# Optimization experiments

Hardware: AMD Instinct MI355X
Metric: run time of the kernel (lower is better)

## Reference

```python
import jax, jax.numpy as jnp
import numpy as np

T = 1024
H_DIM = 2048
VOCAB = 32000
N_EXPERTS = 8
TOP_K = 2
MOE_I = 1024
SHARED_I = 1024
N_HEADS = 16
Q_LORA = 512
KV_LORA = 256
NOPE = 64
ROPE = 32
V_D = 64
EPS = 1e-6
ROUTED_SCALE = 2.5
NEG = -1e30


def rmsnorm(x, w, eps=EPS):
    return x * jax.lax.rsqrt(jnp.mean(x * x, axis=-1, keepdims=True) + eps) * w


def rope_cos_sin(positions):
    inv_freq = 1.0 / (10000.0 ** (jnp.arange(0, ROPE, 2, dtype=jnp.float32) / ROPE))
    freqs = positions.astype(jnp.float32)[:, None] * inv_freq  # [T, ROPE//2]
    return jnp.cos(freqs), jnp.sin(freqs)


def apply_rope(x, cos, sin):
    # interleaved (non-neox) rotary, as DeepSeek MLA uses
    x1, x2 = x[..., 0::2], x[..., 1::2]
    return jnp.stack([x1 * cos - x2 * sin, x1 * sin + x2 * cos], axis=-1).reshape(x.shape)


def setup_inputs() -> dict:
    key = jax.random.key(0)
    ks = jax.random.split(key, 26)
    s = 0.02

    def w(k, shape, scale=s):
        return jax.random.normal(k, shape, dtype=jnp.float32) * scale

    return {
        'input_ids': jax.random.randint(ks[0], (T,), 0, VOCAB, dtype=jnp.int32),
        'positions': jnp.arange(T, dtype=jnp.int32),
        'previous_hidden_states': jax.random.normal(ks[1], (T, H_DIM), dtype=jnp.float32),
        'embed': w(ks[2], (VOCAB, H_DIM), 1.0),
        'enorm_w': jnp.ones((H_DIM,), jnp.float32),
        'hnorm_w': jnp.ones((H_DIM,), jnp.float32),
        'eh_proj_w': w(ks[3], (2 * H_DIM, H_DIM)),
        'in_ln_w': jnp.ones((H_DIM,), jnp.float32),
        'post_ln_w': jnp.ones((H_DIM,), jnp.float32),
        'q_a_w': w(ks[4], (H_DIM, Q_LORA)),
        'q_a_ln_w': jnp.ones((Q_LORA,), jnp.float32),
        'q_b_w': w(ks[5], (Q_LORA, N_HEADS * (NOPE + ROPE))),
        'kv_a_w': w(ks[6], (H_DIM, KV_LORA + ROPE)),
        'kv_a_ln_w': jnp.ones((KV_LORA,), jnp.float32),
        'kv_b_w': w(ks[7], (KV_LORA, N_HEADS * (NOPE + V_D))),
        'o_w': w(ks[8], (N_HEADS * V_D, H_DIM)),
        'gate_w': w(ks[9], (H_DIM, N_EXPERTS)),
        'gate_bias': w(ks[10], (N_EXPERTS,), 0.01),
        'expert_gate_w': w(ks[11], (N_EXPERTS, H_DIM, MOE_I)),
        'expert_up_w': w(ks[12], (N_EXPERTS, H_DIM, MOE_I)),
        'expert_down_w': w(ks[13], (N_EXPERTS, MOE_I, H_DIM)),
        'shared_gate_w': w(ks[14], (H_DIM, SHARED_I)),
        'shared_up_w': w(ks[15], (H_DIM, SHARED_I)),
        'shared_down_w': w(ks[16], (SHARED_I, H_DIM)),
    }


def reference(input_ids, positions, previous_hidden_states, embed, enorm_w, hnorm_w,
              eh_proj_w, in_ln_w, post_ln_w, q_a_w, q_a_ln_w, q_b_w, kv_a_w, kv_a_ln_w,
              kv_b_w, o_w, gate_w, gate_bias, expert_gate_w, expert_up_w, expert_down_w,
              shared_gate_w, shared_up_w, shared_down_w):
    # --- MTP head: RMSNorm x2 + concat + linear ---
    e = embed[input_ids]                                         # [T, h]
    cat_in = jnp.concatenate([rmsnorm(e, enorm_w),
                              rmsnorm(previous_hidden_states, hnorm_w)], axis=-1)
    x0 = cat_in @ eh_proj_w                                      # [T, h]

    # --- decoder layer: MLA attention ---
    resid = x0
    h = rmsnorm(x0, in_ln_w)
    q_a = rmsnorm(h @ q_a_w, q_a_ln_w)                           # [T, q_lora]
    q = (q_a @ q_b_w).reshape(T, N_HEADS, NOPE + ROPE)
    q_nope, q_pe = q[..., :NOPE], q[..., NOPE:]
    kv_a = h @ kv_a_w                                            # [T, kv_lora+rope]
    kv_c, k_pe = kv_a[:, :KV_LORA], kv_a[:, KV_LORA:]
    kv = (rmsnorm(kv_c, kv_a_ln_w) @ kv_b_w).reshape(T, N_HEADS, NOPE + V_D)
    k_nope, v = kv[..., :NOPE], kv[..., NOPE:]
    cos, sin = rope_cos_sin(positions)                           # [T, ROPE//2]
    q_pe = apply_rope(q_pe, cos[:, None, :], sin[:, None, :])
    k_pe = apply_rope(k_pe, cos, sin)
    qf = jnp.concatenate([q_nope, q_pe], axis=-1)                # [T, H, dq]
    kf = jnp.concatenate([k_nope,
                          jnp.broadcast_to(k_pe[:, None, :], (T, N_HEADS, ROPE))], axis=-1)
    scale = (NOPE + ROPE) ** -0.5
    scores = jnp.einsum('thd,shd->hts', qf, kf) * scale          # [H, T, T]
    causal = positions[:, None] >= positions[None, :]
    scores = jnp.where(causal[None], scores, NEG)
    probs = jax.nn.softmax(scores, axis=-1)
    o = jnp.einsum('hts,shv->thv', probs, v).reshape(T, N_HEADS * V_D)
    attn_out = o @ o_w

    resid = resid + attn_out
    h2 = rmsnorm(resid, post_ln_w)

    # --- DeepSeek-V3 MoE: sigmoid gating + bias-corrected top-k ---
    logits = h2 @ gate_w                                         # [T, E]
    sig = jax.nn.sigmoid(logits)
    _, top_idx = jax.lax.top_k(sig + gate_bias, TOP_K)           # selection uses bias
    top_w = jnp.take_along_axis(sig, top_idx, axis=1)            # weights from raw scores
    top_w = top_w / (jnp.sum(top_w, axis=-1, keepdims=True) + 1e-20)
    combine = (jax.nn.one_hot(top_idx, N_EXPERTS, dtype=h2.dtype)
               * top_w[..., None]).sum(axis=1) * ROUTED_SCALE    # [T, E]
    g = jnp.einsum('th,ehi->tei', h2, expert_gate_w)
    u = jnp.einsum('th,ehi->tei', h2, expert_up_w)
    d = jnp.einsum('tei,eih->teh', jax.nn.silu(g) * u, expert_down_w)
    routed = jnp.einsum('teh,te->th', d, combine)
    shared = (jax.nn.silu(h2 @ shared_gate_w) * (h2 @ shared_up_w)) @ shared_down_w
    mlp_out = routed + shared

    # module returns mtp_hidden + mtp_residual
    return mlp_out + resid
```

## Files before the change

kernel.cpp:

```cpp
#include <hip/hip_runtime.h>
#include <hip/hip_bf16.h>
#include <math.h>

constexpr int T_ = 1024;
constexpr int HDIM = 2048;
constexpr int NH = 16;
constexpr int QKD = 96;
constexpr int VD = 64;
constexpr int MAXTILES = 32;
constexpr float EPSF = 1e-6f;

using f32x4 = __attribute__((ext_vector_type(4))) float;
using s16x8 = __attribute__((ext_vector_type(8))) short;
using s16x4 = __attribute__((ext_vector_type(4))) short;

constexpr size_t OF_CATH  = 0;
constexpr size_t OF_CATL  = 2097152;
constexpr size_t OF_X0    = 4194304;
constexpr size_t OF_MACT  = 6291456;
constexpr size_t OF_HH    = 8388608;
constexpr size_t OF_HL    = 9437184;
constexpr size_t OF_QBUF  = 11010048;
constexpr size_t OF_KVBUF = 12877824;
constexpr size_t OF_QAH   = 14974976;
constexpr size_t OF_QAL   = 15237120;
constexpr size_t OF_KVCNH = 15499264;
constexpr size_t OF_KVCNL = 15630336;
constexpr size_t OF_QFH   = 15761408;
constexpr size_t OF_QFL   = 16547840;
constexpr size_t OF_KFH   = 17334272;
constexpr size_t OF_KFL   = 18120704;
constexpr size_t OF_VBH   = 18907136;
constexpr size_t OF_VBL   = 19431424;
constexpr size_t OF_OBH   = 19955712;
constexpr size_t OF_OBL   = 20480000;
constexpr size_t OF_ATT   = 21004288;
constexpr size_t OF_H2BF  = 23101440;
constexpr size_t OF_ROUT  = 24674304;
constexpr size_t OF_EHTH  = 24682752;
constexpr size_t OF_EHTL  = 28877056;
constexpr size_t OF_QBTH  = 34119936;
constexpr size_t OF_QBTL  = 34513152;
constexpr size_t OF_KVBTH = 35561728;
constexpr size_t OF_KVBTL = 35823872;
constexpr size_t OF_OWTH  = 36086016;
constexpr size_t OF_OWTL  = 37134592;
constexpr size_t OF_MD    = 38183168;
constexpr size_t OF_QKRAW = 44474624;
constexpr size_t OF_BATH  = 45293824;
constexpr size_t OF_BATL  = 46145792;

__device__ __forceinline__ short f2bf(float f) {
    union { float f; unsigned u; } x; x.f = f;
    unsigned r = x.u + 0x7fffu + ((x.u >> 16) & 1u);
    return (short)(r >> 16);
}
__device__ __forceinline__ float bf2f(short h) {
    union { unsigned u; float f; } x; x.u = ((unsigned)(unsigned short)h) << 16; return x.f;
}
__device__ __forceinline__ int swz(int r, int k) {
    return (r << 6) + ((((k >> 3) ^ (r & 7)) << 3) | (k & 7));
}
__device__ __forceinline__ void gload16(const void* g, void* l) {
    __builtin_amdgcn_global_load_lds((__attribute__((address_space(1))) void*)g,
                                     (__attribute__((address_space(3))) void*)l, 16, 0, 0);
}

__device__ __forceinline__ float block_sum(float v) {
    __shared__ float sbuf[9];
    int lane = threadIdx.x & 63;
    int wid  = threadIdx.x >> 6;
#pragma unroll
    for (int off = 32; off > 0; off >>= 1) v += __shfl_down(v, off);
    __syncthreads();
    if (lane == 0) sbuf[wid] = v;
    __syncthreads();
    if (threadIdx.x == 0) {
        float s = 0.f;
        int nw = blockDim.x >> 6;
        for (int i = 0; i < nw; i++) s += sbuf[i];
        sbuf[8] = s;
    }
    __syncthreads();
    return sbuf[8];
}

struct TJobs {
    const float* W[6];
    short* Whi[6];
    short* Wlo[6];
    int K[6];
    int N[6];
    int nbx[6];
    int base[7];
};

__global__ void transpose_multi_kernel(TJobs J) {
    int bid = blockIdx.x;
    int j = 0;
#pragma unroll
    for (int i = 1; i < 6; i++) if (bid >= J.base[i]) j = i;
    int local = bid - J.base[j];
    int K = J.K[j], N = J.N[j];
    int bx = local % J.nbx[j], by = local / J.nbx[j];
    const float* W = J.W[j];
    short* Whi = J.Whi[j];
    short* Wlo = J.Wlo[j];

    __shared__ float tile[64][65];
    int k0 = bx * 64, n0 = by * 64;
    int tn = threadIdx.x & 63;
    int tk4 = threadIdx.x >> 6;
#pragma unroll 4
    for (int i = 0; i < 16; i++) {
        int kk = tk4 * 16 + i;
        int gn = n0 + tn;
        tile[kk][tn] = (gn < N) ? W[(size_t)(k0 + kk) * N + gn] : 0.f;
    }
    __syncthreads();
    int on = threadIdx.x >> 2;
    int oc = threadIdx.x & 3;
#pragma unroll 4
    for (int i = 0; i < 16; i++) {
        int kk = oc * 16 + i;
        float v = tile[kk][on];
        short hh = f2bf(v);
        size_t o = (size_t)(n0 + on) * K + k0 + kk;
        Whi[o] = hh;
        Wlo[o] = f2bf(v - bf2f(hh));
    }
}

__global__ void embed_cat_kernel(const int* __restrict__ ids, const float* __restrict__ embed,
                                 const float* __restrict__ enorm, const float* __restrict__ prev,
                                 const float* __restrict__ hnorm, short* __restrict__ ch,
                                 short* __restrict__ cl) {
    int t = blockIdx.x;
    const float* e = embed + (size_t)ids[t] * HDIM;
    float ss = 0.f;
    for (int i = threadIdx.x; i < HDIM; i += blockDim.x) { float v = e[i]; ss += v * v; }
    float r = rsqrtf(block_sum(ss) / HDIM + EPSF);
    for (int i = threadIdx.x; i < HDIM; i += blockDim.x) {
        float v = e[i] * r * enorm[i];
        short hh = f2bf(v);
        ch[(size_t)t * 4096 + i] = hh;
        cl[(size_t)t * 4096 + i] = f2bf(v - bf2f(hh));
    }
    const float* p = prev + (size_t)t * HDIM;
    ss = 0.f;
    for (int i = threadIdx.x; i < HDIM; i += blockDim.x) { float v = p[i]; ss += v * v; }
    r = rsqrtf(block_sum(ss) / HDIM + EPSF);
    for (int i = threadIdx.x; i < HDIM; i += blockDim.x) {
        float v = p[i] * r * hnorm[i];
        short hh = f2bf(v);
        ch[(size_t)t * 4096 + 2048 + i] = hh;
        cl[(size_t)t * 4096 + 2048 + i] = f2bf(v - bf2f(hh));
    }
}

__global__ void rmsnorm_kernel(const float* __restrict__ in, int in_stride, int width,
                               const float* __restrict__ w, float* __restrict__ outf,
                               short* __restrict__ outh, short* __restrict__ outl, int out_stride) {
    int t = blockIdx.x;
    const float* x = in + (size_t)t * in_stride;
    float ss = 0.f;
    for (int i = threadIdx.x; i < width; i += blockDim.x) { float v = x[i]; ss += v * v; }
    float r = rsqrtf(block_sum(ss) / width + EPSF);
    size_t ob = (size_t)t * out_stride;
    for (int i = threadIdx.x; i < width; i += blockDim.x) {
        float v = x[i] * r * w[i];
        if (outf) outf[ob + i] = v;
        if (outh) {
            short hh = f2bf(v);
            outh[ob + i] = hh;
            if (outl) outl[ob + i] = f2bf(v - bf2f(hh));
        }
    }
}

__global__ void rmsnorm_qkv_kernel(const float* __restrict__ qkraw, const float* __restrict__ wq,
                                   const float* __restrict__ wkv, short* __restrict__ qaH,
                                   short* __restrict__ qaL, short* __restrict__ kvcnH,
                                   short* __restrict__ kvcnL) {
    int t = blockIdx.x;
    const float* row = qkraw + (size_t)t * 800;
    float ss = 0.f;
    for (int i = threadIdx.x; i < 512; i += blockDim.x) { float v = row[i]; ss += v * v; }
    float r = rsqrtf(block_sum(ss) / 512.f + EPSF);
    for (int i = threadIdx.x; i < 512; i += blockDim.x) {
        float v = row[i] * r * wq[i];
        short hh = f2bf(v);
        qaH[(size_t)t * 512 + i] = hh;
        qaL[(size_t)t * 512 + i] = f2bf(v - bf2f(hh));
    }
    ss = 0.f;
    for (int i = threadIdx.x; i < 256; i += blockDim.x) { float v = row[512 + i]; ss += v * v; }
    r = rsqrtf(block_sum(ss) / 256.f + EPSF);
    for (int i = threadIdx.x; i < 256; i += blockDim.x) {
        float v = row[512 + i] * r * wkv[i];
        short hh = f2bf(v);
        kvcnH[(size_t)t * 256 + i] = hh;
        kvcnL[(size_t)t * 256 + i] = f2bf(v - bf2f(hh));
    }
}

template<bool SPLIT>
__global__ __launch_bounds__(256) void gemm_planes(const short* __restrict__ Ahi, const short* __restrict__ Alo,
                                                   const short* __restrict__ Bhi, const short* __restrict__ Blo,
                                                   float* __restrict__ C, int M, int N, int K) {
    __shared__ short As[SPLIT ? 2 : 1][128 * 64];
    __shared__ short Bs[SPLIT ? 2 : 1][64 * 64];
    const int tid = threadIdx.x;
    const int lane = tid & 63, wid = tid >> 6;
    const int g = lane >> 4, li = lane & 15;
    const int wm = wid >> 1, wn = wid & 1;
    const int row0 = blockIdx.y * 128, col0 = blockIdx.x * 64;

    f32x4 acc[4][2];
#pragma unroll
    for (int mi = 0; mi < 4; mi++)
#pragma unroll
        for (int ni = 0; ni < 2; ni++)
#pragma unroll
            for (int r = 0; r < 4; r++) acc[mi][ni][r] = 0.f;

    for (int k0 = 0; k0 < K; k0 += 64) {
#pragma unroll
        for (int j = 0; j < 4; j++) {
            int blkI = wid * 4 + j;
            int cid = blkI * 64 + lane;
            int r = cid >> 3, c = (cid & 7) ^ (r & 7);
            gload16(&Ahi[(size_t)(row0 + r) * K + k0 + c * 8], &As[0][blkI * 512]);
            if constexpr (SPLIT)
                gload16(&Alo[(size_t)(row0 + r) * K + k0 + c * 8], &As[1][blkI * 512]);
        }
#pragma unroll
        for (int j = 0; j < 2; j++) {
            int blkI = wid * 2 + j;
            int cid = blkI * 64 + lane;
            int r = cid >> 3, c = (cid & 7) ^ (r & 7);
            gload16(&Bhi[(size_t)(col0 + r) * K + k0 + c * 8], &Bs[0][blkI * 512]);
            if constexpr (SPLIT)
                gload16(&Blo[(size_t)(col0 + r) * K + k0 + c * 8], &Bs[1][blkI * 512]);
        }
        __syncthreads();
#pragma unroll
        for (int kk = 0; kk < 64; kk += 32) {
            s16x8 ah[4], bh[2];
#pragma unroll
            for (int mi = 0; mi < 4; mi++) ah[mi] = *(const s16x8*)&As[0][swz(wm * 64 + mi * 16 + li, kk + g * 8)];
#pragma unroll
            for (int ni = 0; ni < 2; ni++) bh[ni] = *(const s16x8*)&Bs[0][swz(wn * 32 + ni * 16 + li, kk + g * 8)];
            if constexpr (SPLIT) {
                s16x8 al[4], bl[2];
#pragma unroll
                for (int mi = 0; mi < 4; mi++) al[mi] = *(const s16x8*)&As[1][swz(wm * 64 + mi * 16 + li, kk + g * 8)];
#pragma unroll
                for (int ni = 0; ni < 2; ni++) bl[ni] = *(const s16x8*)&Bs[1][swz(wn * 32 + ni * 16 + li, kk + g * 8)];
#pragma unroll
                for (int mi = 0; mi < 4; mi++)
#pragma unroll
                    for (int ni = 0; ni < 2; ni++) {
                        acc[mi][ni] = __builtin_amdgcn_mfma_f32_16x16x32_bf16(ah[mi], bh[ni], acc[mi][ni], 0, 0, 0);
                        acc[mi][ni] = __builtin_amdgcn_mfma_f32_16x16x32_bf16(al[mi], bh[ni], acc[mi][ni], 0, 0, 0);
                        acc[mi][ni] = __builtin_amdgcn_mfma_f32_16x16x32_bf16(ah[mi], bl[ni], acc[mi][ni], 0, 0, 0);
                    }
            } else {
#pragma unroll
                for (int mi = 0; mi < 4; mi++)
#pragma unroll
                    for (int ni = 0; ni < 2; ni++)
                        acc[mi][ni] = __builtin_amdgcn_mfma_f32_16x16x32_bf16(ah[mi], bh[ni], acc[mi][ni], 0, 0, 0);
            }
        }
        __syncthreads();
    }
#pragma unroll
    for (int mi = 0; mi < 4; mi++)
#pragma unroll
        for (int ni = 0; ni < 2; ni++) {
            int gc = col0 + wn * 32 + ni * 16 + li;
            if (gc < N) {
#pragma unroll
                for (int r = 0; r < 4; r++) {
                    int gr = row0 + wm * 64 + mi * 16 + g * 4 + r;
                    C[(size_t)gr * N + gc] = acc[mi][ni][r];
                }
            }
        }
}

__global__ __launch_bounds__(512) void moe_gateup(const short* __restrict__ h2bf, const int* __restrict__ sorted_t,
                                                  const float* __restrict__ Wg, const float* __restrict__ Wu,
                                                  const float* __restrict__ Sg, const float* __restrict__ Su,
                                                  short* __restrict__ Cact, const int4* __restrict__ tilemap,
                                                  int K, int N) {
    int4 tm = tilemap[blockIdx.y];
    int nrows = tm.z;
    if (nrows == 0) return;
    const float* Bg = (tm.x < 8) ? Wg + (size_t)tm.x * K * N : Sg;
    const float* Bu = (tm.x < 8) ? Wu + (size_t)tm.x * K * N : Su;

    __shared__ short As[256 * 64];
    alignas(16) __shared__ short Bgs[64][72];
    alignas(16) __shared__ short Bus[64][72];
    const int tid = threadIdx.x;
    const int lane = tid & 63, wid = tid >> 6;
    const int g = lane >> 4, li = lane & 15;
    const int wm = wid >> 1, wn = wid & 1;
    const int col0 = blockIdx.x * 64;

    int tokens[4];
#pragma unroll
    for (int j = 0; j < 4; j++) {
        int blkI = wid * 4 + j;
        int cid = blkI * 64 + lane;
        int r = cid >> 3;
        int slot = tm.y + r;
        tokens[j] = (slot < 2048) ? sorted_t[slot] : (slot - 2048);
    }

    f32x4 accg[4][2], accu[4][2];
#pragma unroll
    for (int mi = 0; mi < 4; mi++)
#pragma unroll
        for (int ni = 0; ni < 2; ni++)
#pragma unroll
            for (int r = 0; r < 4; r++) { accg[mi][ni][r] = 0.f; accu[mi][ni][r] = 0.f; }

    const int t2 = tid & 255;
    const int skb = (t2 >> 4) << 2, snb = (t2 & 15) << 2;

    for (int k0 = 0; k0 < K; k0 += 64) {
#pragma unroll
        for (int j = 0; j < 4; j++) {
            int blkI = wid * 4 + j;
            int cid = blkI * 64 + lane;
            int r = cid >> 3, c = (cid & 7) ^ (r & 7);
            gload16(&h2bf[(size_t)tokens[j] * K + k0 + c * 8], &As[blkI * 512]);
        }
        {
            const float* B = (tid < 256) ? Bg : Bu;
            short (*Bst)[72] = (tid < 256) ? Bgs : Bus;
            float4 r4[4];
#pragma unroll
            for (int kk = 0; kk < 4; kk++)
                r4[kk] = *(const float4*)(B + (size_t)(k0 + skb + kk) * N + col0 + snb);
#pragma unroll
            for (int n = 0; n < 4; n++) {
                s16x4 w4;
                w4[0] = f2bf((&r4[0].x)[n]); w4[1] = f2bf((&r4[1].x)[n]);
                w4[2] = f2bf((&r4[2].x)[n]); w4[3] = f2bf((&r4[3].x)[n]);
                *(s16x4*)&Bst[snb + n][skb] = w4;
            }
        }
        __syncthreads();
#pragma unroll
        for (int kk = 0; kk < 64; kk += 32) {
            s16x8 a[4], bg2[2], bu2[2];
#pragma unroll
            for (int mi = 0; mi < 4; mi++) a[mi] = *(const s16x8*)&As[swz(wm * 64 + mi * 16 + li, kk + g * 8)];
#pragma unroll
            for (int ni = 0; ni < 2; ni++) {
                bg2[ni] = *(const s16x8*)&Bgs[wn * 32 + ni * 16 + li][kk + g * 8];
                bu2[ni] = *(const s16x8*)&Bus[wn * 32 + ni * 16 + li][kk + g * 8];
            }
#pragma unroll
            for (int mi = 0; mi < 4; mi++)
#pragma unroll
                for (int ni = 0; ni < 2; ni++) {
                    accg[mi][ni] = __builtin_amdgcn_mfma_f32_16x16x32_bf16(a[mi], bg2[ni], accg[mi][ni], 0, 0, 0);
                    accu[mi][ni] = __builtin_amdgcn_mfma_f32_16x16x32_bf16(a[mi], bu2[ni], accu[mi][ni], 0, 0, 0);
                }
        }
        __syncthreads();
    }
#pragma unroll
    for (int mi = 0; mi < 4; mi++)
#pragma unroll
        for (int ni = 0; ni < 2; ni++) {
            int gc = col0 + wn * 32 + ni * 16 + li;
#pragma unroll
            for (int r = 0; r < 4; r++) {
                int gr = wm * 64 + mi * 16 + g * 4 + r;
                if (gr < nrows) {
                    float x = accg[mi][ni][r], u = accu[mi][ni][r];
                    Cact[(size_t)(tm.y + gr) * N + gc] = f2bf((x / (1.f + expf(-x))) * u);
                }
            }
        }
}

__global__ __launch_bounds__(512) void moe_down(const short* __restrict__ Abase, const float* __restrict__ Wall,
                                                const float* __restrict__ Sd, float* __restrict__ Cbase,
                                                const int4* __restrict__ tilemap, int K, int N) {
    int4 tm = tilemap[blockIdx.y];
    int nrows = tm.z;
    if (nrows == 0) return;
    const short* A = Abase + (size_t)tm.y * K;
    float* C = Cbase + (size_t)tm.y * N;
    const float* B = (tm.x < 8) ? Wall + (size_t)tm.x * K * N : Sd;

    __shared__ short As[256 * 64];
    alignas(16) __shared__ short Bs[64][72];
    const int tid = threadIdx.x;
    const int lane = tid & 63, wid = tid >> 6;
    const int g = lane >> 4, li = lane & 15;
    const int wm = wid >> 1, wn = wid & 1;
    const int col0 = blockIdx.x * 64;

    f32x4 acc[4][2];
#pragma unroll
    for (int mi = 0; mi < 4; mi++)
#pragma unroll
        for (int ni = 0; ni < 2; ni++)
#pragma unroll
            for (int r = 0; r < 4; r++) acc[mi][ni][r] = 0.f;

    const int skb = (tid >> 4) << 2, snb = (tid & 15) << 2;

    for (int k0 = 0; k0 < K; k0 += 64) {
#pragma unroll
        for (int j = 0; j < 4; j++) {
            int blkI = wid * 4 + j;
            int cid = blkI * 64 + lane;
            int r = cid >> 3, c = (cid & 7) ^ (r & 7);
            gload16(&A[(size_t)r * K + k0 + c * 8], &As[blkI * 512]);
        }
        if (tid < 256) {
            float4 r4[4];
#pragma unroll
            for (int kk = 0; kk < 4; kk++)
                r4[kk] = *(const float4*)(B + (size_t)(k0 + skb + kk) * N + col0 + snb);
#pragma unroll
            for (int n = 0; n < 4; n++) {
                s16x4 w4;
                w4[0] = f2bf((&r4[0].x)[n]); w4[1] = f2bf((&r4[1].x)[n]);
                w4[2] = f2bf((&r4[2].x)[n]); w4[3] = f2bf((&r4[3].x)[n]);
                *(s16x4*)&Bs[snb + n][skb] = w4;
            }
        }
        __syncthreads();
#pragma unroll
        for (int kk = 0; kk < 64; kk += 32) {
            s16x8 a[4], b[2];
#pragma unroll
            for (int mi = 0; mi < 4; mi++) a[mi] = *(const s16x8*)&As[swz(wm * 64 + mi * 16 + li, kk + g * 8)];
#pragma unroll
            for (int ni = 0; ni < 2; ni++) b[ni] = *(const s16x8*)&Bs[wn * 32 + ni * 16 + li][kk + g * 8];
#pragma unroll
            for (int mi = 0; mi < 4; mi++)
#pragma unroll
                for (int ni = 0; ni < 2; ni++)
                    acc[mi][ni] = __builtin_amdgcn_mfma_f32_16x16x32_bf16(a[mi], b[ni], acc[mi][ni], 0, 0, 0);
        }
        __syncthreads();
    }
#pragma unroll
    for (int mi = 0; mi < 4; mi++)
#pragma unroll
        for (int ni = 0; ni < 2; ni++) {
            int gc = col0 + wn * 32 + ni * 16 + li;
#pragma unroll
            for (int r = 0; r < 4; r++) {
                int gr = wm * 64 + mi * 16 + g * 4 + r;
                if (gr < nrows) C[(size_t)gr * N + gc] = acc[mi][ni][r];
            }
        }
}

__global__ void prep_qkv_kernel(const float* __restrict__ q, const float* __restrict__ qkraw,
                                const float* __restrict__ kv, const int* __restrict__ positions,
                                short* __restrict__ qfh, short* __restrict__ qfl,
                                short* __restrict__ kfh, short* __restrict__ kfl,
                                short* __restrict__ vbh, short* __restrict__ vbl) {
    int t = blockIdx.x;
    __shared__ float cs[16], sn[16];
    if (threadIdx.x < 16) {
        float invf = powf(10000.f, -(float)(2 * threadIdx.x) / 32.f);
        float fr = (float)positions[t] * invf;
        cs[threadIdx.x] = cosf(fr);
        sn[threadIdx.x] = sinf(fr);
    }
    __syncthreads();
    for (int i = threadIdx.x; i < NH * QKD; i += blockDim.x) {
        int h = i / QKD, d = i % QKD;
        float val;
        if (d < 64) val = q[(size_t)t * 1536 + h * QKD + d];
        else {
            int r = d - 64, pr = r >> 1;
            float x1 = q[(size_t)t * 1536 + h * QKD + 64 + 2 * pr];
            float x2 = q[(size_t)t * 1536 + h * QKD + 64 + 2 * pr + 1];
            val = (r & 1) ? (x1 * sn[pr] + x2 * cs[pr]) : (x1 * cs[pr] - x2 * sn[pr]);
        }
        short hh = f2bf(val);
        qfh[(size_t)t * 1536 + i] = hh;
        qfl[(size_t)t * 1536 + i] = f2bf(val - bf2f(hh));
    }
    for (int i = threadIdx.x; i < NH * QKD; i += blockDim.x) {
        int h = i / QKD, d = i % QKD;
        float val;
        if (d < 64) val = kv[(size_t)t * 2048 + h * 128 + d];
        else {
            int r = d - 64, pr = r >> 1;
            float x1 = qkraw[(size_t)t * 800 + 768 + 2 * pr];
            float x2 = qkraw[(size_t)t * 800 + 768 + 2 * pr + 1];
            val = (r & 1) ? (x1 * sn[pr] + x2 * cs[pr]) : (x1 * cs[pr] - x2 * sn[pr]);
        }
        short hh = f2bf(val);
        kfh[(size_t)t * 1536 + i] = hh;
        kfl[(size_t)t * 1536 + i] = f2bf(val - bf2f(hh));
    }
    for (int i = threadIdx.x; i < NH * VD; i += blockDim.x) {
        int h = i / VD, d = i % VD;
        float val = kv[(size_t)t * 2048 + h * 128 + 64 + d];
        short hh = f2bf(val);
        vbh[(size_t)t * 1024 + i] = hh;
        vbl[(size_t)t * 1024 + i] = f2bf(val - bf2f(hh));
    }
}

__global__ __launch_bounds__(256) void attn_mfma_kernel(const short* __restrict__ qfh, const short* __restrict__ qfl,
                                                        const short* __restrict__ kfh, const short* __restrict__ kfl,
                                                        const short* __restrict__ vbh, const short* __restrict__ vbl,
                                                        short* __restrict__ obh, short* __restrict__ obl) {
    __shared__ short K_hi[64][104], K_lo[64][104];
    __shared__ short Vt_hi[64][72], Vt_lo[64][72];
    __shared__ short P_hi[4][16][72], P_lo[4][16][72];
    const int qt = blockIdx.x, h = blockIdx.y;
    const int tid = threadIdx.x, lane = tid & 63, w = tid >> 6;
    const int g = lane >> 4, li = lane & 15;

    s16x8 q_hi[3], q_lo[3];
    {
        const short* qb_h = qfh + (size_t)(qt * 64 + w * 16 + li) * 1536 + h * QKD;
        const short* qb_l = qfl + (size_t)(qt * 64 + w * 16 + li) * 1536 + h * QKD;
#pragma unroll
        for (int ks = 0; ks < 3; ks++) {
            q_hi[ks] = *(const s16x8*)(qb_h + ks * 32 + g * 8);
            q_lo[ks] = *(const s16x8*)(qb_l + ks * 32 + g * 8);
        }
    }

    f32x4 acc_o[4];
#pragma unroll
    for (int nc = 0; nc < 4; nc++)
#pragma unroll
        for (int r = 0; r < 4; r++) acc_o[nc][r] = 0.f;
    float m4[4] = {-1e30f, -1e30f, -1e30f, -1e30f};
    float l4[4] = {0.f, 0.f, 0.f, 0.f};
    const float scale = 0.102062072616f;

    for (int kt = 0; kt <= qt; kt++) {
#pragma unroll
        for (int it = 0; it < 3; it++) {
            int cid = it * 256 + tid;
            int key = cid / 12, c = cid % 12;
            *(s16x8*)&K_hi[key][c * 8] = *(const s16x8*)&kfh[(size_t)(kt * 64 + key) * 1536 + h * QKD + c * 8];
            *(s16x8*)&K_lo[key][c * 8] = *(const s16x8*)&kfl[(size_t)(kt * 64 + key) * 1536 + h * QKD + c * 8];
        }
#pragma unroll
        for (int it = 0; it < 2; it++) {
            int cid = it * 256 + tid;
            int key = cid >> 3, vc = cid & 7;
            s16x8 vh = *(const s16x8*)&vbh[(size_t)(kt * 64 + key) * 1024 + h * VD + vc * 8];
            s16x8 vl = *(const s16x8*)&vbl[(size_t)(kt * 64 + key) * 1024 + h * VD + vc * 8];
#pragma unroll
            for (int j = 0; j < 8; j++) {
                Vt_hi[vc * 8 + j][key] = vh[j];
                Vt_lo[vc * 8 + j][key] = vl[j];
            }
        }
        __syncthreads();

        f32x4 acc_s[4];
#pragma unroll
        for (int kc = 0; kc < 4; kc++)
#pragma unroll
            for (int r = 0; r < 4; r++) acc_s[kc][r] = 0.f;
#pragma unroll
        for (int ks = 0; ks < 3; ks++) {
#pragma unroll
            for (int kc = 0; kc < 4; kc++) {
                s16x8 kh = *(const s16x8*)&K_hi[kc * 16 + li][ks * 32 + g * 8];
                s16x8 kl = *(const s16x8*)&K_lo[kc * 16 + li][ks * 32 + g * 8];
                acc_s[kc] = __builtin_amdgcn_mfma_f32_16x16x32_bf16(q_hi[ks], kh, acc_s[kc], 0, 0, 0);
                acc_s[kc] = __builtin_amdgcn_mfma_f32_16x16x32_bf16(q_lo[ks], kh, acc_s[kc], 0, 0, 0);
                acc_s[kc] = __builtin_amdgcn_mfma_f32_16x16x32_bf16(q_hi[ks], kl, acc_s[kc], 0, 0, 0);
            }
        }
#pragma unroll
        for (int kc = 0; kc < 4; kc++)
#pragma unroll
            for (int r = 0; r < 4; r++) acc_s[kc][r] *= scale;
        if (kt == qt) {
#pragma unroll
            for (int kc = 0; kc < 4; kc++) {
                int key = kt * 64 + kc * 16 + li;
#pragma unroll
                for (int r = 0; r < 4; r++) {
                    int qr = qt * 64 + w * 16 + g * 4 + r;
                    if (key > qr) acc_s[kc][r] = -1e30f;
                }
            }
        }
        float tm4[4];
#pragma unroll
        for (int r = 0; r < 4; r++)
            tm4[r] = fmaxf(fmaxf(acc_s[0][r], acc_s[1][r]), fmaxf(acc_s[2][r], acc_s[3][r]));
#pragma unroll
        for (int off = 1; off < 16; off <<= 1)
#pragma unroll
            for (int r = 0; r < 4; r++) tm4[r] = fmaxf(tm4[r], __shfl_xor(tm4[r], off));
        float alpha[4];
#pragma unroll
        for (int r = 0; r < 4; r++) {
            float mn = fmaxf(m4[r], tm4[r]);
            alpha[r] = __expf(m4[r] - mn);
            m4[r] = mn;
        }
        float rs[4] = {0.f, 0.f, 0.f, 0.f};
#pragma unroll
        for (int kc = 0; kc < 4; kc++)
#pragma unroll
            for (int r = 0; r < 4; r++) {
                float p = __expf(acc_s[kc][r] - m4[r]);
                rs[r] += p;
                short hh = f2bf(p);
                P_hi[w][g * 4 + r][kc * 16 + li] = hh;
                P_lo[w][g * 4 + r][kc * 16 + li] = f2bf(p - bf2f(hh));
            }
#pragma unroll
        for (int off = 1; off < 16; off <<= 1)
#pragma unroll
            for (int r = 0; r < 4; r++) rs[r] += __shfl_xor(rs[r], off);
#pragma unroll
        for (int r = 0; r < 4; r++) l4[r] = l4[r] * alpha[r] + rs[r];
#pragma unroll
        for (int nc = 0; nc < 4; nc++)
#pragma unroll
            for (int r = 0; r < 4; r++) acc_o[nc][r] *= alpha[r];
#pragma unroll
        for (int ks = 0; ks < 2; ks++) {
            s16x8 ph = *(const s16x8*)&P_hi[w][li][ks * 32 + g * 8];
            s16x8 pl = *(const s16x8*)&P_lo[w][li][ks * 32 + g * 8];
#pragma unroll
            for (int nc = 0; nc < 4; nc++) {
                s16x8 vh = *(const s16x8*)&Vt_hi[nc * 16 + li][ks * 32 + g * 8];
                s16x8 vl = *(const s16x8*)&Vt_lo[nc * 16 + li][ks * 32 + g * 8];
                acc_o[nc] = __builtin_amdgcn_mfma_f32_16x16x32_bf16(ph, vh, acc_o[nc], 0, 0, 0);
                acc_o[nc] = __builtin_amdgcn_mfma_f32_16x16x32_bf16(pl, vh, acc_o[nc], 0, 0, 0);
                acc_o[nc] = __builtin_amdgcn_mfma_f32_16x16x32_bf16(ph, vl, acc_o[nc], 0, 0, 0);
            }
        }
        __syncthreads();
    }
    float inv[4];
#pragma unroll
    for (int r = 0; r < 4; r++) inv[r] = 1.f / l4[r];
#pragma unroll
    for (int nc = 0; nc < 4; nc++)
#pragma unroll
        for (int r = 0; r < 4; r++) {
            float o = acc_o[nc][r] * inv[r];
            size_t idx = (size_t)(qt * 64 + w * 16 + g * 4 + r) * 1024 + h * VD + nc * 16 + li;
            short hh = f2bf(o);
            obh[idx] = hh;
            obl[idx] = f2bf(o - bf2f(hh));
        }
}

__global__ __launch_bounds__(256) void fused_post_attn(float* __restrict__ x0, const float* __restrict__ att,
                                                       const float* __restrict__ w, const float* __restrict__ gate_w,
                                                       const float* __restrict__ gate_bias,
                                                       short* __restrict__ h2bf, int* __restrict__ topidx,
                                                       float* __restrict__ topw) {
    int t = blockIdx.x;
    float resid[8];
    float ss = 0.f;
#pragma unroll
    for (int j = 0; j < 8; j++) {
        int i = threadIdx.x + j * 256;
        float v = x0[(size_t)t * HDIM + i] + att[(size_t)t * HDIM + i];
        resid[j] = v;
        x0[(size_t)t * HDIM + i] = v;
        ss += v * v;
    }
    float r = rsqrtf(block_sum(ss) / HDIM + EPSF);
    float acc[8] = {0.f, 0.f, 0.f, 0.f, 0.f, 0.f, 0.f, 0.f};
#pragma unroll
    for (int j = 0; j < 8; j++) {
        int i = threadIdx.x + j * 256;
        float v = resid[j] * r * w[i];
        h2bf[(size_t)t * HDIM + i] = f2bf(v);
        const float* gw = gate_w + (size_t)i * 8;
        float4 g0 = *(const float4*)gw;
        float4 g1 = *(const float4*)(gw + 4);
        acc[0] = fmaf(v, g0.x, acc[0]); acc[1] = fmaf(v, g0.y, acc[1]);
        acc[2] = fmaf(v, g0.z, acc[2]); acc[3] = fmaf(v, g0.w, acc[3]);
        acc[4] = fmaf(v, g1.x, acc[4]); acc[5] = fmaf(v, g1.y, acc[5]);
        acc[6] = fmaf(v, g1.z, acc[6]); acc[7] = fmaf(v, g1.w, acc[7]);
    }
    __shared__ float logits[8];
    for (int e = 0; e < 8; e++) {
        float s = block_sum(acc[e]);
        if (threadIdx.x == 0) logits[e] = s;
    }
    __syncthreads();
    if (threadIdx.x == 0) {
        float sig[8], sc[8];
        for (int e = 0; e < 8; e++) {
            sig[e] = 1.f / (1.f + expf(-logits[e]));
            sc[e] = sig[e] + gate_bias[e];
        }
        int i0 = 0;
        for (int e = 1; e < 8; e++) if (sc[e] > sc[i0]) i0 = e;
        int i1 = -1;
        for (int e = 0; e < 8; e++) if (e != i0 && (i1 < 0 || sc[e] > sc[i1])) i1 = e;
        float w0 = sig[i0], w1 = sig[i1], s = w0 + w1 + 1e-20f;
        topidx[t * 2 + 0] = i0; topidx[t * 2 + 1] = i1;
        topw[t * 2 + 0] = w0 / s; topw[t * 2 + 1] = w1 / s;
    }
}

__global__ void sort_kernel(const int* __restrict__ topidx, int* __restrict__ sorted_t,
                            int* __restrict__ slotpos, int4* __restrict__ tilemap) {
    __shared__ int counts[8], offs[9];
    int wid = threadIdx.x >> 6, lane = threadIdx.x & 63;
    int cnt = 0;
    for (int base = 0; base < 2 * T_; base += 64) {
        int e = topidx[base + lane];
        unsigned long long m = __ballot(e == wid);
        cnt += __popcll(m);
    }
    if (lane == 0) counts[wid] = cnt;
    __syncthreads();
    if (threadIdx.x == 0) {
        offs[0] = 0;
        for (int e = 0; e < 8; e++) offs[e + 1] = offs[e] + counts[e];
    }
    __syncthreads();
    int pos = offs[wid];
    for (int base = 0; base < 2 * T_; base += 64) {
        int sl = base + lane;
        int e = topidx[sl];
        bool match = (e == wid);
        unsigned long long m = __ballot(match);
        if (match) {
            int before = __popcll(m & ((1ull << lane) - 1ull));
            int pp = pos + before;
            sorted_t[pp] = sl >> 1;
            slotpos[sl] = pp;
        }
        pos += __popcll(m);
    }
    __syncthreads();
    if (threadIdx.x == 0) {
        int nt = 0;
        for (int e = 0; e < 8; e++) {
            int c = counts[e], o = offs[e];
            for (int r = 0; r < c; r += 256) {
                tilemap[nt] = make_int4(e, o + r, min(256, c - r), 0);
                nt++;
            }
        }
        for (int r = 0; r < 4; r++) {
            tilemap[nt] = make_int4(8, 2048 + r * 256, 256, 0);
            nt++;
        }
        for (int i = nt; i < MAXTILES; i++) tilemap[i] = make_int4(0, 0, 0, 0);
    }
}

__global__ void final_kernel(const float* __restrict__ resid, const float* __restrict__ md,
                             const int* __restrict__ slotpos, const float* __restrict__ topw,
                             float* __restrict__ out) {
    int t = blockIdx.x;
    int p0 = slotpos[t * 2 + 0], p1 = slotpos[t * 2 + 1];
    float w0 = topw[t * 2 + 0] * 2.5f, w1 = topw[t * 2 + 1] * 2.5f;
    const float* mds = md + (size_t)(2048 + t) * HDIM;
    for (int c = threadIdx.x; c < HDIM; c += blockDim.x) {
        float v = resid[(size_t)t * HDIM + c] + mds[c]
                + w0 * md[(size_t)p0 * HDIM + c] + w1 * md[(size_t)p1 * HDIM + c];
        out[(size_t)t * HDIM + c] = v;
    }
}

extern "C" void kernel_launch(void* const* d_in, const int* in_sizes, int n_in,
                              void* d_out, int out_size, void* d_ws, size_t ws_size,
                              hipStream_t stream) {
    (void)in_sizes; (void)n_in; (void)out_size; (void)ws_size;
    const int*   input_ids = (const int*)d_in[0];
    const int*   positions = (const int*)d_in[1];
    const float* prev      = (const float*)d_in[2];
    const float* embed     = (const float*)d_in[3];
    const float* enorm_w   = (const float*)d_in[4];
    const float* hnorm_w   = (const float*)d_in[5];
    const float* eh_proj_w = (const float*)d_in[6];
    const float* in_ln_w   = (const float*)d_in[7];
    const float* post_ln_w = (const float*)d_in[8];
    const float* q_a_w     = (const float*)d_in[9];
    const float* q_a_ln_w  = (const float*)d_in[10];
    const float* q_b_w     = (const float*)d_in[11];
    const float* kv_a_w    = (const float*)d_in[12];
    const float* kv_a_ln_w = (const float*)d_in[13];
    const float* kv_b_w    = (const float*)d_in[14];
    const float* o_w       = (const float*)d_in[15];
    const float* gate_w    = (const float*)d_in[16];
    const float* gate_bias = (const float*)d_in[17];
    const float* exp_g     = (const float*)d_in[18];
    const float* exp_u     = (const float*)d_in[19];
    const float* exp_d     = (const float*)d_in[20];
    const float* sh_g      = (const float*)d_in[21];
    const float* sh_u      = (const float*)d_in[22];
    const float* sh_d      = (const float*)d_in[23];
    float* out = (float*)d_out;

    float* ws = (float*)d_ws;
    short* catH  = (short*)(ws + OF_CATH);
    short* catL  = (short*)(ws + OF_CATL);
    float* x0    = ws + OF_X0;
    short* mact  = (short*)(ws + OF_MACT);
    short* hH    = (short*)(ws + OF_HH);
    short* hL    = (short*)(ws + OF_HL);
    float* qbuf  = ws + OF_QBUF;
    float* kvbuf = ws + OF_KVBUF;
    short* qaH   = (short*)(ws + OF_QAH);
    short* qaL   = (short*)(ws + OF_QAL);
    short* kvcnH = (short*)(ws + OF_KVCNH);
    short* kvcnL = (short*)(ws + OF_KVCNL);
    short* qfH   = (short*)(ws + OF_QFH);
    short* qfL   = (short*)(ws + OF_QFL);
    short* kfH   = (short*)(ws + OF_KFH);
    short* kfL   = (short*)(ws + OF_KFL);
    short* vbH   = (short*)(ws + OF_VBH);
    short* vbL   = (short*)(ws + OF_VBL);
    short* obH   = (short*)(ws + OF_OBH);
    short* obL   = (short*)(ws + OF_OBL);
    float* att   = ws + OF_ATT;
    short* h2bf  = (short*)(ws + OF_H2BF);
    float* md    = ws + OF_MD;
    float* qkraw = ws + OF_QKRAW;
    short* batH  = (short*)(ws + OF_BATH);
    short* batL  = (short*)(ws + OF_BATL);
    int*   ri       = (int*)(ws + OF_ROUT);
    int*   topidx   = ri;
    int*   sorted_t = ri + 2048;
    int*   slotpos  = ri + 4096;
    int4*  tilemap  = (int4*)(ri + 6144);
    float* topw     = (float*)(ri + 6144 + 4 * MAXTILES);
    short* ehTH  = (short*)(ws + OF_EHTH);
    short* ehTL  = (short*)(ws + OF_EHTL);
    short* qbTH  = (short*)(ws + OF_QBTH);
    short* qbTL  = (short*)(ws + OF_QBTL);
    short* kvbTH = (short*)(ws + OF_KVBTH);
    short* kvbTL = (short*)(ws + OF_KVBTL);
    short* owTH  = (short*)(ws + OF_OWTH);
    short* owTL  = (short*)(ws + OF_OWTL);

    dim3 blk(256);

    TJobs J;
    J.W[0] = eh_proj_w; J.Whi[0] = ehTH; J.Wlo[0] = ehTL; J.K[0] = 4096; J.N[0] = 2048; J.nbx[0] = 64;
    J.W[1] = q_a_w; J.Whi[1] = batH; J.Wlo[1] = batL; J.K[1] = 2048; J.N[1] = 512; J.nbx[1] = 32;
    J.W[2] = kv_a_w; J.Whi[2] = batH + (size_t)512 * 2048; J.Wlo[2] = batL + (size_t)512 * 2048;
    J.K[2] = 2048; J.N[2] = 288; J.nbx[2] = 32;
    J.W[3] = q_b_w; J.Whi[3] = qbTH; J.Wlo[3] = qbTL; J.K[3] = 512; J.N[3] = 1536; J.nbx[3] = 8;
    J.W[4] = kv_b_w; J.Whi[4] = kvbTH; J.Wlo[4] = kvbTL; J.K[4] = 256; J.N[4] = 2048; J.nbx[4] = 4;
    J.W[5] = o_w; J.Whi[5] = owTH; J.Wlo[5] = owTL; J.K[5] = 1024; J.N[5] = 2048; J.nbx[5] = 16;
    int nby[6] = {32, 8, 5, 24, 32, 32};
    J.base[0] = 0;
    for (int i = 0; i < 6; i++) J.base[i + 1] = J.base[i] + J.nbx[i] * nby[i];
    transpose_multi_kernel<<<J.base[6], blk, 0, stream>>>(J);

    embed_cat_kernel<<<T_, blk, 0, stream>>>(input_ids, embed, enorm_w, prev, hnorm_w, catH, catL);
    gemm_planes<true><<<dim3(32, 8), blk, 0, stream>>>(catH, catL, ehTH, ehTL, x0, T_, 2048, 4096);
    rmsnorm_kernel<<<T_, blk, 0, stream>>>(x0, 2048, 2048, in_ln_w, nullptr, hH, hL, 2048);
    gemm_planes<true><<<dim3(13, 8), blk, 0, stream>>>(hH, hL, batH, batL, qkraw, T_, 800, 2048);
    rmsnorm_qkv_kernel<<<T_, blk, 0, stream>>>(qkraw, q_a_ln_w, kv_a_ln_w, qaH, qaL, kvcnH, kvcnL);
    gemm_planes<true><<<dim3(24, 8), blk, 0, stream>>>(qaH, qaL, qbTH, qbTL, qbuf, T_, 1536, 512);
    gemm_planes<true><<<dim3(32, 8), blk, 0, stream>>>(kvcnH, kvcnL, kvbTH, kvbTL, kvbuf, T_, 2048, 256);
    prep_qkv_kernel<<<T_, blk, 0, stream>>>(qbuf, qkraw, kvbuf, positions, qfH, qfL, kfH, kfL, vbH, vbL);
    attn_mfma_kernel<<<dim3(T_ / 64, NH), blk, 0, stream>>>(qfH, qfL, kfH, kfL, vbH, vbL, obH, obL);
    gemm_planes<true><<<dim3(32, 8), blk, 0, stream>>>(obH, obL, owTH, owTL, att, T_, 2048, 1024);
    fused_post_attn<<<T_, blk, 0, stream>>>(x0, att, post_ln_w, gate_w, gate_bias, h2bf, topidx, topw);
    sort_kernel<<<1, 512, 0, stream>>>(topidx, sorted_t, slotpos, tilemap);
    moe_gateup<<<dim3(16, MAXTILES), dim3(512), 0, stream>>>(h2bf, sorted_t, exp_g, exp_u, sh_g, sh_u, mact, tilemap, 2048, 1024);
    moe_down<<<dim3(32, MAXTILES), dim3(512), 0, stream>>>(mact, exp_d, sh_d, md, tilemap, 1024, 2048);
    final_kernel<<<T_, blk, 0, stream>>>(x0, md, slotpos, topw, out);
}
```

Before: 516.8 us.

## Split long causal attention rows into two KV halves with a combine pass

```diff
diff --git a/kernel.cpp b/kernel.cpp
--- a/kernel.cpp
+++ b/kernel.cpp
@@ -8,6 +8,7 @@
 constexpr int QKD = 96;
 constexpr int VD = 64;
 constexpr int MAXTILES = 32;
+constexpr int NITEMS = 24;
 constexpr float EPSF = 1e-6f;
 
 using f32x4 = __attribute__((ext_vector_type(4))) float;
@@ -49,6 +50,8 @@
 constexpr size_t OF_QKRAW = 44474624;
 constexpr size_t OF_BATH  = 45293824;
 constexpr size_t OF_BATL  = 46145792;
+constexpr size_t OF_OPART = 46997760;
+constexpr size_t OF_MLPART= 49094912;
 
 __device__ __forceinline__ short f2bf(float f) {
     union { float f; unsigned u; } x; x.f = f;
@@ -523,11 +526,24 @@
 __global__ __launch_bounds__(256) void attn_mfma_kernel(const short* __restrict__ qfh, const short* __restrict__ qfl,
                                                         const short* __restrict__ kfh, const short* __restrict__ kfl,
                                                         const short* __restrict__ vbh, const short* __restrict__ vbl,
-                                                        short* __restrict__ obh, short* __restrict__ obl) {
+                                                        short* __restrict__ obh, short* __restrict__ obl,
+                                                        float* __restrict__ o_part, float* __restrict__ ml_part) {
     __shared__ short K_hi[64][104], K_lo[64][104];
     __shared__ short Vt_hi[64][72], Vt_lo[64][72];
     __shared__ short P_hi[4][16][72], P_lo[4][16][72];
-    const int qt = blockIdx.x, h = blockIdx.y;
+    const int item = blockIdx.x, h = blockIdx.y;
+    int qt, kt0, kt1, part;
+    bool full;
+    if (item < 8) { qt = item; kt0 = 0; kt1 = qt + 1; full = true; part = 0; }
+    else {
+        int i = item - 8;
+        qt = 8 + (i >> 1);
+        part = i & 1;
+        int mid = (qt + 1) >> 1;
+        full = false;
+        kt0 = part ? mid : 0;
+        kt1 = part ? (qt + 1) : mid;
+    }
     const int tid = threadIdx.x, lane = tid & 63, w = tid >> 6;
     const int g = lane >> 4, li = lane & 15;
 
@@ -551,7 +567,7 @@
     float l4[4] = {0.f, 0.f, 0.f, 0.f};
     const float scale = 0.102062072616f;
 
-    for (int kt = 0; kt <= qt; kt++) {
+    for (int kt = kt0; kt < kt1; kt++) {
 #pragma unroll
         for (int it = 0; it < 3; it++) {
             int cid = it * 256 + tid;
@@ -655,19 +671,64 @@
         }
         __syncthreads();
     }
-    float inv[4];
-#pragma unroll
-    for (int r = 0; r < 4; r++) inv[r] = 1.f / l4[r];
-#pragma unroll
-    for (int nc = 0; nc < 4; nc++)
-#pragma unroll
-        for (int r = 0; r < 4; r++) {
-            float o = acc_o[nc][r] * inv[r];
-            size_t idx = (size_t)(qt * 64 + w * 16 + g * 4 + r) * 1024 + h * VD + nc * 16 + li;
-            short hh = f2bf(o);
-            obh[idx] = hh;
-            obl[idx] = f2bf(o - bf2f(hh));
-        }
+    if (full) {
+        float inv[4];
+#pragma unroll
+        for (int r = 0; r < 4; r++) inv[r] = 1.f / l4[r];
+#pragma unroll
+        for (int nc = 0; nc < 4; nc++)
+#pragma unroll
+            for (int r = 0; r < 4; r++) {
+                float o = acc_o[nc][r] * inv[r];
+                size_t idx = (size_t)(qt * 64 + w * 16 + g * 4 + r) * 1024 + h * VD + nc * 16 + li;
+                short hh = f2bf(o);
+                obh[idx] = hh;
+                obl[idx] = f2bf(o - bf2f(hh));
+            }
+    } else {
+#pragma unroll
+        for (int nc = 0; nc < 4; nc++)
+#pragma unroll
+            for (int r = 0; r < 4; r++) {
+                int t = qt * 64 + w * 16 + g * 4 + r;
+                o_part[(((size_t)part * 1024 + t) * 16 + h) * 64 + nc * 16 + li] = acc_o[nc][r];
+            }
+        if (li == 0) {
+#pragma unroll
+            for (int r = 0; r < 4; r++) {
+                int t = qt * 64 + w * 16 + g * 4 + r;
+                size_t o = (((size_t)part * 1024 + t) * 16 + h) * 2;
+                ml_part[o] = m4[r];
+                ml_part[o + 1] = l4[r];
+            }
+        }
+    }
+}
+
+__global__ __launch_bounds__(256) void attn_combine_kernel(const float* __restrict__ o_part,
+                                                           const float* __restrict__ ml_part,
+                                                           short* __restrict__ obh, short* __restrict__ obl) {
+    int t = 512 + blockIdx.x;
+    int idx4 = threadIdx.x * 4;
+    int h = idx4 >> 6;
+    int vd = idx4 & 63;
+    size_t mb0 = (((size_t)0 * 1024 + t) * 16 + h) * 2;
+    size_t mb1 = (((size_t)1 * 1024 + t) * 16 + h) * 2;
+    float m0 = ml_part[mb0], l0 = ml_part[mb0 + 1];
+    float m1 = ml_part[mb1], l1 = ml_part[mb1 + 1];
+    float ms = fmaxf(m0, m1);
+    float a0 = __expf(m0 - ms), a1 = __expf(m1 - ms);
+    float inv = 1.f / (l0 * a0 + l1 * a1);
+    size_t b0 = (((size_t)0 * 1024 + t) * 16 + h) * 64 + vd;
+    size_t b1 = (((size_t)1 * 1024 + t) * 16 + h) * 64 + vd;
+#pragma unroll
+    for (int j = 0; j < 4; j++) {
+        float o = (o_part[b0 + j] * a0 + o_part[b1 + j] * a1) * inv;
+        size_t oi = (size_t)t * 1024 + h * VD + vd + j;
+        short hh = f2bf(o);
+        obh[oi] = hh;
+        obl[oi] = f2bf(o - bf2f(hh));
+    }
 }
 
 __global__ __launch_bounds__(256) void fused_post_attn(float* __restrict__ x0, const float* __restrict__ att,
@@ -843,6 +904,8 @@
     float* qkraw = ws + OF_QKRAW;
     short* batH  = (short*)(ws + OF_BATH);
     short* batL  = (short*)(ws + OF_BATL);
+    float* opart = ws + OF_OPART;
+    float* mlpart= ws + OF_MLPART;
     int*   ri       = (int*)(ws + OF_ROUT);
     int*   topidx   = ri;
     int*   sorted_t = ri + 2048;
@@ -881,7 +944,8 @@
     gemm_planes<true><<<dim3(24, 8), blk, 0, stream>>>(qaH, qaL, qbTH, qbTL, qbuf, T_, 1536, 512);
     gemm_planes<true><<<dim3(32, 8), blk, 0, stream>>>(kvcnH, kvcnL, kvbTH, kvbTL, kvbuf, T_, 2048, 256);
     prep_qkv_kernel<<<T_, blk, 0, stream>>>(qbuf, qkraw, kvbuf, positions, qfH, qfL, kfH, kfL, vbH, vbL);
-    attn_mfma_kernel<<<dim3(T_ / 64, NH), blk, 0, stream>>>(qfH, qfL, kfH, kfL, vbH, vbL, obH, obL);
+    attn_mfma_kernel<<<dim3(NITEMS, NH), blk, 0, stream>>>(qfH, qfL, kfH, kfL, vbH, vbL, obH, obL, opart, mlpart);
+    attn_combine_kernel<<<512, blk, 0, stream>>>(opart, mlpart, obH, obL);
     gemm_planes<true><<<dim3(32, 8), blk, 0, stream>>>(obH, obL, owTH, owTL, att, T_, 2048, 1024);
     fused_post_attn<<<T_, blk, 0, stream>>>(x0, att, post_ln_w, gate_w, gate_bias, h2bf, topidx, topw);
     sort_kernel<<<1, 512, 0, stream>>>(topidx, sorted_t, slotpos, tilemap);
```

After: 508.7 us. About the same (-1.6%).
